# Kernel optimization log

Measured on AMD Instinct MI355X. Metric: run time of the kernel, lower is better.

Reference implementation:

```python
import jax, jax.numpy as jnp
import numpy as np

B, H, T, K, V = 2, 8, 2048, 128, 128


def setup_inputs() -> dict:
    key = jax.random.key(0)
    k1, k2, k3, k4, k5 = jax.random.split(key, 5)
    return {
        "q": jax.random.normal(k1, (B, H, T, K), dtype=jnp.float32),
        "k": jax.random.normal(k2, (B, H, T, K), dtype=jnp.float32),
        "v": jax.random.normal(k3, (B, H, T, V), dtype=jnp.float32),
        "i_gate": jax.random.normal(k4, (B, H, T), dtype=jnp.float32),
        "f_gate": jax.random.normal(k5, (B, H, T), dtype=jnp.float32),
    }


def reference(q, k, v, i_gate, f_gate):
    # Stabilized parallel mLSTM (same math as the chunked Triton kernel,
    # expressed in natural-log base instead of base-2).
    Bq, Hq, Tq, Kd = q.shape
    scale = Kd ** -0.5
    logf = jax.nn.log_sigmoid(f_gate)                      # [B,H,T]
    fc = jnp.cumsum(logf, axis=-1)                         # cumulative forget logits
    # log decay matrix: logD[t,s] = i[s] + (fc[t] - fc[s]) for s <= t
    logD = fc[..., :, None] - fc[..., None, :] + i_gate[..., None, :]  # [B,H,T,T]
    mask = jnp.tril(jnp.ones((Tq, Tq), dtype=bool))
    logD_masked = jnp.where(mask, logD, -jnp.inf)
    m = jnp.max(logD_masked, axis=-1)                      # row-wise stabilizer [B,H,T]
    D = jnp.where(mask, jnp.exp(logD - m[..., None]), 0.0) # stabilized decay matrix
    S = jnp.einsum("bhtk,bhsk->bhts", q, k) * scale * D    # gated scores
    norm = jnp.maximum(jnp.abs(jnp.sum(S, axis=-1)), jnp.exp(-m))  # [B,H,T]
    h = jnp.einsum("bhts,bhsv->bhtv", S, v) / norm[..., None]
    return h
```

## Files before the change

kernel.cpp:

```cpp
#include <hip/hip_runtime.h>

#define T_SEQ 2048
#define DHEAD 128
#define NBH 16
#define SCALE 0.08838834764831845f

typedef unsigned short u16;
typedef unsigned int u32;
typedef u16 u16x4 __attribute__((ext_vector_type(4)));
typedef u16 u16x8 __attribute__((ext_vector_type(8)));
typedef u32 u32x2 __attribute__((ext_vector_type(2)));
typedef short s16x4 __attribute__((ext_vector_type(4)));
typedef __bf16 bf16x8 __attribute__((ext_vector_type(8)));
typedef float f32x4 __attribute__((ext_vector_type(4)));

__device__ __forceinline__ u16 f2bfu(float x) {
  union { float f; unsigned u; } c; c.f = x;
  unsigned u = c.u;
  u = u + 0x7FFFu + ((u >> 16) & 1u);
  return (u16)(u >> 16);
}

__device__ __forceinline__ u32 packbf2(float lo, float hi) {
  return (u32)f2bfu(lo) | ((u32)f2bfu(hi) << 16);
}

__device__ __forceinline__ bf16x8 ldsFrag(const u16* p) {
  u16x8 t = *(const u16x8*)p;
  return __builtin_bit_cast(bf16x8, t);
}

__device__ __forceinline__ f32x4 mfma16x16x16bf16(s16x4 a, s16x4 b, f32x4 c) {
#if __has_builtin(__builtin_amdgcn_mfma_f32_16x16x16bf16_1k)
  return __builtin_amdgcn_mfma_f32_16x16x16bf16_1k(a, b, c, 0, 0, 0);
#else
  asm("v_mfma_f32_16x16x16_bf16 %0, %1, %2, %0" : "+v"(c) : "v"(a), "v"(b));
  return c;
#endif
}

__device__ __forceinline__ void gld_lds16(const void* g, void* l) {
  __builtin_amdgcn_global_load_lds(
      (__attribute__((address_space(1))) const unsigned int*)g,
      (__attribute__((address_space(3))) unsigned int*)l, 16, 0, 0);
}

__global__ __launch_bounds__(1024) void gate_scan_kernel(
    const float* __restrict__ ig, const float* __restrict__ fg,
    float* __restrict__ a_out, float* __restrict__ c_out,
    float* __restrict__ fc_out)
{
  const int bh = blockIdx.x, tid = threadIdx.x;
  const int w = tid >> 6, lane = tid & 63;
  const int base = bh * T_SEQ + tid * 2;
  __shared__ float wsum[16];
  __shared__ float wmax[16];

  const float x0 = fg[base], x1 = fg[base + 1];
  const float ls0 = fminf(x0, 0.f) - log1pf(expf(-fabsf(x0)));
  const float ls1 = fminf(x1, 0.f) - log1pf(expf(-fabsf(x1)));
  const float s = ls0 + ls1;

  float sc = s;
#pragma unroll
  for (int off = 1; off < 64; off <<= 1) {
    const float t = __shfl_up(sc, off, 64);
    if (lane >= off) sc += t;
  }
  if (lane == 63) wsum[w] = sc;
  __syncthreads();
  float wo = 0.f;
#pragma unroll
  for (int i = 0; i < 15; ++i) if (i < w) wo += wsum[i];
  const float excl = wo + (sc - s);
  const float fc0 = excl + ls0;
  const float fc1 = excl + ls0 + ls1;
  fc_out[base] = fc0; fc_out[base + 1] = fc1;
  const float a0 = ig[base] - fc0;
  const float a1 = ig[base + 1] - fc1;
  a_out[base] = a0; a_out[base + 1] = a1;

  const float m = fmaxf(a0, a1);
  float mc = m;
#pragma unroll
  for (int off = 1; off < 64; off <<= 1) {
    const float t = __shfl_up(mc, off, 64);
    if (lane >= off) mc = fmaxf(mc, t);
  }
  if (lane == 63) wmax[w] = mc;
  __syncthreads();
  float wmo = -INFINITY;
#pragma unroll
  for (int i = 0; i < 15; ++i) if (i < w) wmo = fmaxf(wmo, wmax[i]);
  const float prev = __shfl_up(mc, 1, 64);
  float exclm = (lane > 0) ? prev : -INFINITY;
  exclm = fmaxf(exclm, wmo);
  c_out[base] = fmaxf(exclm, a0);
  c_out[base + 1] = fmaxf(exclm, m);
}

__global__ __launch_bounds__(256) void cvt_k_kernel(
    const float* __restrict__ src, const float* __restrict__ ag,
    const float* __restrict__ cg, u16* __restrict__ dst)
{
  const int i = (blockIdx.x * 256 + threadIdx.x) * 4;
  const int bhs = i >> 7;
  const float sc = __expf(ag[bhs] - cg[bhs | 63]);
  const float4 x = *(const float4*)(src + i);
  u16x4 p;
  p[0] = f2bfu(x.x * sc); p[1] = f2bfu(x.y * sc);
  p[2] = f2bfu(x.z * sc); p[3] = f2bfu(x.w * sc);
  *(u16x4*)(dst + i) = p;
}

__global__ __launch_bounds__(256) void cvt_vt_kernel(
    const float* __restrict__ v, u16* __restrict__ vt)
{
  const int bh = blockIdx.y, kt = blockIdx.x, tid = threadIdx.x;
  __shared__ __align__(16) u16 L[128 * 72];
  const int n0 = (tid & 31) * 4, k0 = (tid >> 5) * 8;
  const float* vp = v + ((size_t)bh * T_SEQ + kt * 64 + k0) * DHEAD + n0;
  u16 tv[4][8];
#pragma unroll
  for (int rr = 0; rr < 8; ++rr) {
    const float4 x = *(const float4*)(vp + rr * DHEAD);
    tv[0][rr] = f2bfu(x.x); tv[1][rr] = f2bfu(x.y);
    tv[2][rr] = f2bfu(x.z); tv[3][rr] = f2bfu(x.w);
  }
#pragma unroll
  for (int j = 0; j < 4; ++j) {
    u16x8 p;
#pragma unroll
    for (int rr = 0; rr < 8; ++rr) p[rr] = tv[j][rr];
    *(u16x8*)(&L[(n0 + j) * 72 + k0]) = p;
  }
  __syncthreads();
  const int row = tid >> 1, s0 = (tid & 1) * 32;
  u16* op = vt + ((size_t)bh * DHEAD + row) * T_SEQ + kt * 64 + s0;
#pragma unroll
  for (int i = 0; i < 4; ++i)
    *(u16x8*)(op + i * 8) = *(const u16x8*)(&L[row * 72 + s0 + i * 8]);
}

template <bool FAST>
__global__ __launch_bounds__(1024, 4) void mlstm_fwd_kernel(
    const float* __restrict__ qg, const float* __restrict__ kxg,
    const float* __restrict__ vg,
    const u16* __restrict__ kbf, const u16* __restrict__ vtbf,
    const float* __restrict__ ag, const float* __restrict__ cg,
    const float* __restrict__ fcg, float* __restrict__ out)
{
  const int bx = (int)blockIdx.x;
  const int bh = bx & 15, p = bx >> 4;
  const int tid = (int)threadIdx.x;
  const int w = tid >> 6, lane = tid & 63;
  const int quad = lane >> 4, l16 = lane & 15;
  const int kg = w & 3, rq = w >> 2;

  const int qtA = 31 - p, qtB = p;
  const int nA = qtA + 1;

  __shared__ __align__(16) unsigned char SM[99584];
  u16* Kst = (u16*)SM;
  u16* Vst = (u16*)(SM + 32768);
  float* osh = (float*)(SM + 65536);
  float* rsh = (float*)(SM + 98560);

  const size_t hoff = (size_t)bh * T_SEQ * DHEAD;
  const int goff = bh * T_SEQ;

  bf16x8 qf[4];
  auto loadQ = [&](int lqt) {
    const float* qp = qg + hoff + (size_t)(lqt * 64 + rq * 16 + l16) * DHEAD + quad * 8;
#pragma unroll
    for (int kc = 0; kc < 4; ++kc) {
      const float4 x0 = *(const float4*)(qp + kc * 32);
      const float4 x1 = *(const float4*)(qp + kc * 32 + 4);
      u16x8 t;
      t[0] = f2bfu(x0.x); t[1] = f2bfu(x0.y); t[2] = f2bfu(x0.z); t[3] = f2bfu(x0.w);
      t[4] = f2bfu(x1.x); t[5] = f2bfu(x1.y); t[6] = f2bfu(x1.z); t[7] = f2bfu(x1.w);
      qf[kc] = __builtin_bit_cast(bf16x8, t);
    }
  };

  f32x4 oa[8];
  float rsacc;
  auto zeroAcc = [&]() {
#pragma unroll
    for (int mt = 0; mt < 8; ++mt) oa[mt] = (f32x4){0.f, 0.f, 0.f, 0.f};
    rsacc = 0.f;
  };
  zeroAcc();

  auto stage = [&](int st, int b) {
    u16* KbL = Kst + b * 8192;
    u16* VbL = Vst + b * 8192;
    if (FAST) {
      const u16* ks = kbf + ((size_t)goff + st * 64) * DHEAD;
      const u16* vs = vtbf + (size_t)bh * DHEAD * T_SEQ + st * 64;
      { const int key = tid >> 4; const int db = (tid & 15) ^ (key & 7);
        gld_lds16(ks + (size_t)key * DHEAD + db * 8, KbL + w * 512); }
      { const int n = tid >> 3; const int kb = (tid & 7) ^ (n & 7);
        gld_lds16(vs + (size_t)n * T_SEQ + kb * 8, VbL + w * 512); }
    } else {
      const float ct = cg[goff + st * 64 + 63];
      const float* kp = kxg + hoff + (size_t)(st * 64) * DHEAD;
      const float* vp = vg + hoff + (size_t)(st * 64) * DHEAD;
      { const int key = tid >> 4; const int db = (tid & 15) ^ (key & 7);
        const float sc = __expf(ag[goff + st * 64 + key] - ct);
        const float4 x0 = *(const float4*)(kp + (size_t)key * DHEAD + db * 8);
        const float4 x1 = *(const float4*)(kp + (size_t)key * DHEAD + db * 8 + 4);
        u16x8 pk;
        pk[0] = f2bfu(x0.x * sc); pk[1] = f2bfu(x0.y * sc);
        pk[2] = f2bfu(x0.z * sc); pk[3] = f2bfu(x0.w * sc);
        pk[4] = f2bfu(x1.x * sc); pk[5] = f2bfu(x1.y * sc);
        pk[6] = f2bfu(x1.z * sc); pk[7] = f2bfu(x1.w * sc);
        *(u16x8*)(KbL + tid * 8) = pk; }
      { const int n = tid >> 3; const int kb = (tid & 7) ^ (n & 7);
        u16x8 pw;
#pragma unroll
        for (int rr = 0; rr < 8; ++rr)
          pw[rr] = f2bfu(vp[(size_t)(kb * 8 + rr) * DHEAD + n]);
        *(u16x8*)(VbL + tid * 8) = pw; }
    }
  };

  const int keyA = kg * 16 + l16;
  const int ksw  = l16 & 7;
  const int kbu  = kg * 2 + (quad >> 1);
  const int kofs = (quad & 1) * 4;

  auto computeTile = [&](int cqt, int st, int b, float ccmax) {
    const u16* KbL = Kst + b * 8192;
    const u16* VbL = Vst + b * 8192;

    f32x4 sa = (f32x4){0.f, 0.f, 0.f, 0.f};
#pragma unroll
    for (int kc = 0; kc < 4; ++kc) {
      const bf16x8 kf = ldsFrag(KbL + keyA * 128 + (((kc * 4 + quad) ^ ksw) * 8));
      sa = __builtin_amdgcn_mfma_f32_16x16x32_bf16(kf, qf[kc], sa, 0, 0, 0);
    }

    const float etile = SCALE * __expf(cg[goff + st * 64 + 63] - ccmax);
    float x0 = sa[0] * etile, x1 = sa[1] * etile;
    float x2 = sa[2] * etile, x3 = sa[3] * etile;
    if (st == cqt) {
      const int qr = rq * 16 + l16, kb0 = kg * 16 + quad * 4;
      if (kb0 + 0 > qr) x0 = 0.f;
      if (kb0 + 1 > qr) x1 = 0.f;
      if (kb0 + 2 > qr) x2 = 0.f;
      if (kb0 + 3 > qr) x3 = 0.f;
    }
    rsacc += (x0 + x1) + (x2 + x3);
    const s16x4 pfr = __builtin_bit_cast(s16x4, (u32x2){packbf2(x0, x1), packbf2(x2, x3)});

#pragma unroll
    for (int mt = 0; mt < 8; ++mt) {
      const int vd = mt * 16 + l16;
      const s16x4 va = *(const s16x4*)(VbL + vd * 64 + ((kbu ^ (vd & 7)) * 8) + kofs);
      oa[mt] = mfma16x16x16bf16(va, pfr, oa[mt]);
    }
  };

  auto epilogue = [&](int eqt, float ecmax) {
    float x = rsacc;
    x += __shfl_xor(x, 16, 64);
    x += __shfl_xor(x, 32, 64);
    if (lane < 16) rsh[kg * 64 + rq * 16 + lane] = x;
    __syncthreads();
    float inv = 0.f;
    if (kg == 3) {
      const int row = rq * 16 + l16;
      const float tot = rsh[row] + rsh[64 + row] + rsh[128 + row] + rsh[192 + row];
      const float nf = __expf(-(ecmax + fcg[goff + eqt * 64 + row]));
      inv = 1.f / fmaxf(fabsf(tot), nf);
    }
    for (int r = 0; r < 4; ++r) {
      if (kg == r) {
#pragma unroll
        for (int mt = 0; mt < 8; ++mt)
#pragma unroll
          for (int rg = 0; rg < 4; ++rg) {
            const int row = rq * 16 + l16;
            const int vd = mt * 16 + quad * 4 + rg;
            const int ad = row * 129 + vd;
            float v = oa[mt][rg];
            if (r > 0) v += osh[ad];
            if (r == 3) v *= inv;
            osh[ad] = v;
          }
      }
      __syncthreads();
    }
    const int col = tid & 31, r0 = tid >> 5;
#pragma unroll
    for (int i = 0; i < 2; ++i) {
      const int row = r0 + 32 * i;
      const float* lp = osh + row * 129 + col * 4;
      float4 v; v.x = lp[0]; v.y = lp[1]; v.z = lp[2]; v.w = lp[3];
      *(float4*)(out + hoff + (size_t)(eqt * 64 + row) * DHEAD + col * 4) = v;
    }
  };

  int qt = qtA;
  float cmax = cg[goff + qtA * 64 + 63];
  loadQ(qtA);
  stage(0, 0);
  __syncthreads();

  for (int it = 0; it < 33; ++it) {
    if (it < 32) {
      const int nx = it + 1;
      stage((nx < nA) ? nx : nx - nA, nx & 1);
    }
    computeTile(qt, (it < nA) ? it : it - nA, it & 1, cmax);
    __syncthreads();
    if (it == nA - 1) {
      epilogue(qtA, cmax);
      zeroAcc();
      qt = qtB;
      cmax = cg[goff + qtB * 64 + 63];
      loadQ(qtB);
    }
  }
  epilogue(qtB, cmax);
}

extern "C" void kernel_launch(void* const* d_in, const int* in_sizes, int n_in,
                              void* d_out, int out_size, void* d_ws, size_t ws_size,
                              hipStream_t stream) {
  const float* q  = (const float*)d_in[0];
  const float* k  = (const float*)d_in[1];
  const float* v  = (const float*)d_in[2];
  const float* ig = (const float*)d_in[3];
  const float* fg = (const float*)d_in[4];

  const size_t gate_bytes = (size_t)3 * NBH * T_SEQ * sizeof(float);
  const size_t kv_elems   = (size_t)NBH * T_SEQ * DHEAD;
  const bool fast = ws_size >= gate_bytes + 2 * kv_elems * sizeof(u16);

  float* a_ws  = (float*)d_ws;
  float* c_ws  = a_ws + NBH * T_SEQ;
  float* fc_ws = c_ws + NBH * T_SEQ;
  u16* kbf  = (u16*)((char*)d_ws + gate_bytes);
  u16* vtbf = kbf + kv_elems;

  gate_scan_kernel<<<dim3(NBH), dim3(1024), 0, stream>>>(ig, fg, a_ws, c_ws, fc_ws);
  if (fast) {
    cvt_k_kernel<<<dim3((unsigned)(kv_elems / 1024)), dim3(256), 0, stream>>>(
        k, a_ws, c_ws, kbf);
    cvt_vt_kernel<<<dim3(T_SEQ / 64, NBH), dim3(256), 0, stream>>>(v, vtbf);
    mlstm_fwd_kernel<true><<<dim3(256), dim3(1024), 0, stream>>>(
        q, k, v, kbf, vtbf, a_ws, c_ws, fc_ws, (float*)d_out);
  } else {
    mlstm_fwd_kernel<false><<<dim3(256), dim3(1024), 0, stream>>>(
        q, k, v, kbf, vtbf, a_ws, c_ws, fc_ws, (float*)d_out);
  }
}
```

Measured before the change: 147.1 us.

## Process two key stages per iteration with 32-row Q per wave; fuse K/V conversion

The main kernel now splits its 16 waves into two stage groups that each handle a different 64-key stage, and each wave computes 32 query rows (two MFMA tiles) so every K/V fragment loaded from LDS is used twice. Stages are double-buffered in pairs, which halves the number of barrier-separated iterations, and the epilogue reduces across 8 wave groups using the freed staging buffer. The separate K-scaling and V-transpose conversion kernels are merged into one launch. In exchange, accumulator registers double, LDS use grows to about 130KB, and the cross-wave output reduction takes twice as many serialized steps.

```diff
diff --git a/kernel.cpp b/kernel.cpp
--- a/kernel.cpp
+++ b/kernel.cpp
@@ -99,24 +99,28 @@
   c_out[base + 1] = fmaxf(exclm, m);
 }
 
-__global__ __launch_bounds__(256) void cvt_k_kernel(
-    const float* __restrict__ src, const float* __restrict__ ag,
-    const float* __restrict__ cg, u16* __restrict__ dst)
-{
-  const int i = (blockIdx.x * 256 + threadIdx.x) * 4;
-  const int bhs = i >> 7;
-  const float sc = __expf(ag[bhs] - cg[bhs | 63]);
-  const float4 x = *(const float4*)(src + i);
-  u16x4 p;
-  p[0] = f2bfu(x.x * sc); p[1] = f2bfu(x.y * sc);
-  p[2] = f2bfu(x.z * sc); p[3] = f2bfu(x.w * sc);
-  *(u16x4*)(dst + i) = p;
-}
-
-__global__ __launch_bounds__(256) void cvt_vt_kernel(
-    const float* __restrict__ v, u16* __restrict__ vt)
+__global__ __launch_bounds__(256) void cvt_kv_kernel(
+    const float* __restrict__ kk, const float* __restrict__ v,
+    const float* __restrict__ ag, const float* __restrict__ cg,
+    u16* __restrict__ kbf, u16* __restrict__ vt)
 {
   const int bh = blockIdx.y, kt = blockIdx.x, tid = threadIdx.x;
+  {
+    const int r = tid >> 2;
+    const int c0 = (tid & 3) * 32;
+    const int row = kt * 64 + r;
+    const float sc = __expf(ag[bh * T_SEQ + row] - cg[bh * T_SEQ + (row | 63)]);
+    const float* sp = kk + ((size_t)bh * T_SEQ + row) * DHEAD + c0;
+    u16* dp = kbf + ((size_t)bh * T_SEQ + row) * DHEAD + c0;
+#pragma unroll
+    for (int j = 0; j < 8; ++j) {
+      const float4 x = *(const float4*)(sp + j * 4);
+      u16x4 pq;
+      pq[0] = f2bfu(x.x * sc); pq[1] = f2bfu(x.y * sc);
+      pq[2] = f2bfu(x.z * sc); pq[3] = f2bfu(x.w * sc);
+      *(u16x4*)(dp + j * 4) = pq;
+    }
+  }
   __shared__ __align__(16) u16 L[128 * 72];
   const int n0 = (tid & 31) * 4, k0 = (tid >> 5) * 8;
   const float* vp = v + ((size_t)bh * T_SEQ + kt * 64 + k0) * DHEAD + n0;
@@ -129,10 +133,10 @@
   }
 #pragma unroll
   for (int j = 0; j < 4; ++j) {
-    u16x8 p;
-#pragma unroll
-    for (int rr = 0; rr < 8; ++rr) p[rr] = tv[j][rr];
-    *(u16x8*)(&L[(n0 + j) * 72 + k0]) = p;
+    u16x8 pq;
+#pragma unroll
+    for (int rr = 0; rr < 8; ++rr) pq[rr] = tv[j][rr];
+    *(u16x8*)(&L[(n0 + j) * 72 + k0]) = pq;
   }
   __syncthreads();
   const int row = tid >> 1, s0 = (tid & 1) * 32;
@@ -155,46 +159,48 @@
   const int tid = (int)threadIdx.x;
   const int w = tid >> 6, lane = tid & 63;
   const int quad = lane >> 4, l16 = lane & 15;
-  const int kg = w & 3, rq = w >> 2;
+  const int kg = w & 3, sg = (w >> 2) & 1, rh = w >> 3;
 
   const int qtA = 31 - p, qtB = p;
-  const int nA = qtA + 1;
-
-  __shared__ __align__(16) unsigned char SM[99584];
-  u16* Kst = (u16*)SM;
-  u16* Vst = (u16*)(SM + 32768);
-  float* osh = (float*)(SM + 65536);
-  float* rsh = (float*)(SM + 98560);
+
+  __shared__ __align__(16) unsigned char SM[133376];
+  float* rsh = (float*)(SM + 131072);
+  float* ish = (float*)(SM + 133120);
 
   const size_t hoff = (size_t)bh * T_SEQ * DHEAD;
   const int goff = bh * T_SEQ;
 
-  bf16x8 qf[4];
+  bf16x8 qf[8];
   auto loadQ = [&](int lqt) {
-    const float* qp = qg + hoff + (size_t)(lqt * 64 + rq * 16 + l16) * DHEAD + quad * 8;
-#pragma unroll
-    for (int kc = 0; kc < 4; ++kc) {
-      const float4 x0 = *(const float4*)(qp + kc * 32);
-      const float4 x1 = *(const float4*)(qp + kc * 32 + 4);
-      u16x8 t;
-      t[0] = f2bfu(x0.x); t[1] = f2bfu(x0.y); t[2] = f2bfu(x0.z); t[3] = f2bfu(x0.w);
-      t[4] = f2bfu(x1.x); t[5] = f2bfu(x1.y); t[6] = f2bfu(x1.z); t[7] = f2bfu(x1.w);
-      qf[kc] = __builtin_bit_cast(bf16x8, t);
-    }
-  };
-
-  f32x4 oa[8];
-  float rsacc;
+    const float* qp = qg + hoff + (size_t)(lqt * 64 + rh * 32 + l16) * DHEAD + quad * 8;
+#pragma unroll
+    for (int nt = 0; nt < 2; ++nt)
+#pragma unroll
+      for (int kc = 0; kc < 4; ++kc) {
+        const float4 x0 = *(const float4*)(qp + nt * 16 * DHEAD + kc * 32);
+        const float4 x1 = *(const float4*)(qp + nt * 16 * DHEAD + kc * 32 + 4);
+        u16x8 t;
+        t[0] = f2bfu(x0.x); t[1] = f2bfu(x0.y); t[2] = f2bfu(x0.z); t[3] = f2bfu(x0.w);
+        t[4] = f2bfu(x1.x); t[5] = f2bfu(x1.y); t[6] = f2bfu(x1.z); t[7] = f2bfu(x1.w);
+        qf[nt * 4 + kc] = __builtin_bit_cast(bf16x8, t);
+      }
+  };
+
+  f32x4 oa[8][2];
+  float rs0, rs1;
   auto zeroAcc = [&]() {
 #pragma unroll
-    for (int mt = 0; mt < 8; ++mt) oa[mt] = (f32x4){0.f, 0.f, 0.f, 0.f};
-    rsacc = 0.f;
+    for (int mt = 0; mt < 8; ++mt) {
+      oa[mt][0] = (f32x4){0.f, 0.f, 0.f, 0.f};
+      oa[mt][1] = (f32x4){0.f, 0.f, 0.f, 0.f};
+    }
+    rs0 = 0.f; rs1 = 0.f;
   };
   zeroAcc();
 
-  auto stage = [&](int st, int b) {
-    u16* KbL = Kst + b * 8192;
-    u16* VbL = Vst + b * 8192;
+  auto stage = [&](int st, int slot) {
+    u16* KbL = (u16*)(SM + slot * 32768);
+    u16* VbL = (u16*)(SM + slot * 32768 + 16384);
     if (FAST) {
       const u16* ks = kbf + ((size_t)goff + st * 64) * DHEAD;
       const u16* vs = vtbf + (size_t)bh * DHEAD * T_SEQ + st * 64;
@@ -225,70 +231,106 @@
     }
   };
 
+  auto stagePair = [&](int s0, int lim, int pr) {
+    if (s0 < lim)     stage(s0,     pr * 2);
+    if (s0 + 1 < lim) stage(s0 + 1, pr * 2 + 1);
+  };
+
   const int keyA = kg * 16 + l16;
   const int ksw  = l16 & 7;
   const int kbu  = kg * 2 + (quad >> 1);
   const int kofs = (quad & 1) * 4;
 
-  auto computeTile = [&](int cqt, int st, int b, float ccmax) {
-    const u16* KbL = Kst + b * 8192;
-    const u16* VbL = Vst + b * 8192;
-
-    f32x4 sa = (f32x4){0.f, 0.f, 0.f, 0.f};
+  auto computeStage = [&](int cqt, int st, int slot, float ccmax) {
+    const u16* KbL = (const u16*)(SM + slot * 32768);
+    const u16* VbL = (const u16*)(SM + slot * 32768 + 16384);
+
+    f32x4 sa0 = (f32x4){0.f, 0.f, 0.f, 0.f};
+    f32x4 sa1 = (f32x4){0.f, 0.f, 0.f, 0.f};
 #pragma unroll
     for (int kc = 0; kc < 4; ++kc) {
       const bf16x8 kf = ldsFrag(KbL + keyA * 128 + (((kc * 4 + quad) ^ ksw) * 8));
-      sa = __builtin_amdgcn_mfma_f32_16x16x32_bf16(kf, qf[kc], sa, 0, 0, 0);
+      sa0 = __builtin_amdgcn_mfma_f32_16x16x32_bf16(kf, qf[kc],     sa0, 0, 0, 0);
+      sa1 = __builtin_amdgcn_mfma_f32_16x16x32_bf16(kf, qf[4 + kc], sa1, 0, 0, 0);
     }
 
     const float etile = SCALE * __expf(cg[goff + st * 64 + 63] - ccmax);
-    float x0 = sa[0] * etile, x1 = sa[1] * etile;
-    float x2 = sa[2] * etile, x3 = sa[3] * etile;
-    if (st == cqt) {
-      const int qr = rq * 16 + l16, kb0 = kg * 16 + quad * 4;
-      if (kb0 + 0 > qr) x0 = 0.f;
-      if (kb0 + 1 > qr) x1 = 0.f;
-      if (kb0 + 2 > qr) x2 = 0.f;
-      if (kb0 + 3 > qr) x3 = 0.f;
-    }
-    rsacc += (x0 + x1) + (x2 + x3);
-    const s16x4 pfr = __builtin_bit_cast(s16x4, (u32x2){packbf2(x0, x1), packbf2(x2, x3)});
+    const bool diag = (st == cqt);
+    const int kb0 = kg * 16 + quad * 4;
+
+    s16x4 pfr0, pfr1;
+    {
+      float x0 = sa0[0] * etile, x1 = sa0[1] * etile;
+      float x2 = sa0[2] * etile, x3 = sa0[3] * etile;
+      if (diag) {
+        const int qr = rh * 32 + l16;
+        if (kb0 + 0 > qr) x0 = 0.f;
+        if (kb0 + 1 > qr) x1 = 0.f;
+        if (kb0 + 2 > qr) x2 = 0.f;
+        if (kb0 + 3 > qr) x3 = 0.f;
+      }
+      rs0 += (x0 + x1) + (x2 + x3);
+      pfr0 = __builtin_bit_cast(s16x4, (u32x2){packbf2(x0, x1), packbf2(x2, x3)});
+    }
+    {
+      float x0 = sa1[0] * etile, x1 = sa1[1] * etile;
+      float x2 = sa1[2] * etile, x3 = sa1[3] * etile;
+      if (diag) {
+        const int qr = rh * 32 + 16 + l16;
+        if (kb0 + 0 > qr) x0 = 0.f;
+        if (kb0 + 1 > qr) x1 = 0.f;
+        if (kb0 + 2 > qr) x2 = 0.f;
+        if (kb0 + 3 > qr) x3 = 0.f;
+      }
+      rs1 += (x0 + x1) + (x2 + x3);
+      pfr1 = __builtin_bit_cast(s16x4, (u32x2){packbf2(x0, x1), packbf2(x2, x3)});
+    }
 
 #pragma unroll
     for (int mt = 0; mt < 8; ++mt) {
       const int vd = mt * 16 + l16;
       const s16x4 va = *(const s16x4*)(VbL + vd * 64 + ((kbu ^ (vd & 7)) * 8) + kofs);
-      oa[mt] = mfma16x16x16bf16(va, pfr, oa[mt]);
-    }
-  };
-
-  auto epilogue = [&](int eqt, float ecmax) {
-    float x = rsacc;
-    x += __shfl_xor(x, 16, 64);
-    x += __shfl_xor(x, 32, 64);
-    if (lane < 16) rsh[kg * 64 + rq * 16 + lane] = x;
+      oa[mt][0] = mfma16x16x16bf16(va, pfr0, oa[mt][0]);
+      oa[mt][1] = mfma16x16x16bf16(va, pfr1, oa[mt][1]);
+    }
+  };
+
+  auto epilogue = [&](int eqt, float ecmax, int epair) {
+    float* osh = (float*)(SM + epair * 65536);
+    float x0 = rs0, x1 = rs1;
+    x0 += __shfl_xor(x0, 16, 64); x0 += __shfl_xor(x0, 32, 64);
+    x1 += __shfl_xor(x1, 16, 64); x1 += __shfl_xor(x1, 32, 64);
+    if (lane < 16) {
+      rsh[(w & 7) * 64 + rh * 32 + lane]      = x0;
+      rsh[(w & 7) * 64 + rh * 32 + 16 + lane] = x1;
+    }
     __syncthreads();
-    float inv = 0.f;
-    if (kg == 3) {
-      const int row = rq * 16 + l16;
-      const float tot = rsh[row] + rsh[64 + row] + rsh[128 + row] + rsh[192 + row];
+    if (w == 15) {
+      const int row = lane;
+      float tot = 0.f;
+#pragma unroll
+      for (int j = 0; j < 8; ++j) tot += rsh[j * 64 + row];
       const float nf = __expf(-(ecmax + fcg[goff + eqt * 64 + row]));
-      inv = 1.f / fmaxf(fabsf(tot), nf);
-    }
-    for (int r = 0; r < 4; ++r) {
-      if (kg == r) {
+      ish[row] = 1.f / fmaxf(fabsf(tot), nf);
+    }
+    for (int r = 0; r < 8; ++r) {
+      if ((w & 7) == r) {
+        float iv0 = 0.f, iv1 = 0.f;
+        if (r == 7) { iv0 = ish[rh * 32 + l16]; iv1 = ish[rh * 32 + 16 + l16]; }
 #pragma unroll
         for (int mt = 0; mt < 8; ++mt)
 #pragma unroll
-          for (int rg = 0; rg < 4; ++rg) {
-            const int row = rq * 16 + l16;
-            const int vd = mt * 16 + quad * 4 + rg;
-            const int ad = row * 129 + vd;
-            float v = oa[mt][rg];
-            if (r > 0) v += osh[ad];
-            if (r == 3) v *= inv;
-            osh[ad] = v;
-          }
+          for (int nt = 0; nt < 2; ++nt)
+#pragma unroll
+            for (int rg = 0; rg < 4; ++rg) {
+              const int row = rh * 32 + nt * 16 + l16;
+              const int vd = mt * 16 + quad * 4 + rg;
+              const int ad = row * 129 + vd;
+              float vv = oa[mt][nt][rg];
+              if (r > 0) vv += osh[ad];
+              if (r == 7) vv *= (nt ? iv1 : iv0);
+              osh[ad] = vv;
+            }
       }
       __syncthreads();
     }
@@ -297,33 +339,37 @@
     for (int i = 0; i < 2; ++i) {
       const int row = r0 + 32 * i;
       const float* lp = osh + row * 129 + col * 4;
-      float4 v; v.x = lp[0]; v.y = lp[1]; v.z = lp[2]; v.w = lp[3];
-      *(float4*)(out + hoff + (size_t)(eqt * 64 + row) * DHEAD + col * 4) = v;
-    }
-  };
-
-  int qt = qtA;
+      float4 vv; vv.x = lp[0]; vv.y = lp[1]; vv.z = lp[2]; vv.w = lp[3];
+      *(float4*)(out + hoff + (size_t)(eqt * 64 + row) * DHEAD + col * 4) = vv;
+    }
+    __syncthreads();
+  };
+
+  int qt = qtA, n = qtA + 1;
   float cmax = cg[goff + qtA * 64 + 63];
   loadQ(qtA);
-  stage(0, 0);
+  stagePair(0, n, 0);
   __syncthreads();
 
-  for (int it = 0; it < 33; ++it) {
-    if (it < 32) {
-      const int nx = it + 1;
-      stage((nx < nA) ? nx : nx - nA, nx & 1);
-    }
-    computeTile(qt, (it < nA) ? it : it - nA, it & 1, cmax);
-    __syncthreads();
-    if (it == nA - 1) {
-      epilogue(qtA, cmax);
+  int pair = 0;
+  for (int phase = 0; phase < 2; ++phase) {
+    const int c = (n + 1) >> 1;
+    for (int g = 0; g < c; ++g) {
+      if (g + 1 < c)        stagePair(2 * (g + 1), n, pair ^ 1);
+      else if (phase == 0)  stagePair(0, qtB + 1, pair ^ 1);
+      const int st = 2 * g + sg;
+      if (st < n) computeStage(qt, st, pair * 2 + sg, cmax);
+      __syncthreads();
+      pair ^= 1;
+    }
+    if (phase == 0) loadQ(qtB);
+    epilogue(qt, cmax, pair ^ 1);
+    if (phase == 0) {
       zeroAcc();
-      qt = qtB;
+      qt = qtB; n = qtB + 1;
       cmax = cg[goff + qtB * 64 + 63];
-      loadQ(qtB);
-    }
-  }
-  epilogue(qtB, cmax);
+    }
+  }
 }
 
 extern "C" void kernel_launch(void* const* d_in, const int* in_sizes, int n_in,
@@ -347,9 +393,8 @@
 
   gate_scan_kernel<<<dim3(NBH), dim3(1024), 0, stream>>>(ig, fg, a_ws, c_ws, fc_ws);
   if (fast) {
-    cvt_k_kernel<<<dim3((unsigned)(kv_elems / 1024)), dim3(256), 0, stream>>>(
-        k, a_ws, c_ws, kbf);
-    cvt_vt_kernel<<<dim3(T_SEQ / 64, NBH), dim3(256), 0, stream>>>(v, vtbf);
+    cvt_kv_kernel<<<dim3(T_SEQ / 64, NBH), dim3(256), 0, stream>>>(
+        k, v, a_ws, c_ws, kbf, vtbf);
     mlstm_fwd_kernel<true><<<dim3(256), dim3(1024), 0, stream>>>(
         q, k, v, kbf, vtbf, a_ws, c_ws, fc_ws, (float*)d_out);
   } else {
```

Result: slower. 196.4 us (+33.5%).

## Triple-buffer K/V staging with vmcnt waits and fuse K/V conversion kernels

Applied to the files above, without the earlier changes.

The main kernel moves from double to triple buffering of K/V tiles in LDS. It waits on vmcnt(2) plus a raw s_barrier, so each iteration needs one barrier instead of two syncthreads and the loads stay two tiles ahead. The K scaling/convert and V transpose kernels are merged into one launch. P packing now uses the hardware v_cvt_pk_bf16_f32 instruction, and the epilogue reduction uses vectorised f32x4 LDS accesses with a 132-float padded row. The cost is larger LDS use (133 KB), which limits occupancy, and the manual waitcnt and barrier handling needs care to stay correct.

```diff
diff --git a/kernel.cpp b/kernel.cpp
--- a/kernel.cpp
+++ b/kernel.cpp
@@ -14,15 +14,13 @@
 typedef __bf16 bf16x8 __attribute__((ext_vector_type(8)));
 typedef float f32x4 __attribute__((ext_vector_type(4)));
 
+#define SFENCE() __builtin_amdgcn_sched_barrier(0)
+
 __device__ __forceinline__ u16 f2bfu(float x) {
   union { float f; unsigned u; } c; c.f = x;
   unsigned u = c.u;
   u = u + 0x7FFFu + ((u >> 16) & 1u);
   return (u16)(u >> 16);
-}
-
-__device__ __forceinline__ u32 packbf2(float lo, float hi) {
-  return (u32)f2bfu(lo) | ((u32)f2bfu(hi) << 16);
 }
 
 __device__ __forceinline__ bf16x8 ldsFrag(const u16* p) {
@@ -99,24 +97,28 @@
   c_out[base + 1] = fmaxf(exclm, m);
 }
 
-__global__ __launch_bounds__(256) void cvt_k_kernel(
-    const float* __restrict__ src, const float* __restrict__ ag,
-    const float* __restrict__ cg, u16* __restrict__ dst)
-{
-  const int i = (blockIdx.x * 256 + threadIdx.x) * 4;
-  const int bhs = i >> 7;
-  const float sc = __expf(ag[bhs] - cg[bhs | 63]);
-  const float4 x = *(const float4*)(src + i);
-  u16x4 p;
-  p[0] = f2bfu(x.x * sc); p[1] = f2bfu(x.y * sc);
-  p[2] = f2bfu(x.z * sc); p[3] = f2bfu(x.w * sc);
-  *(u16x4*)(dst + i) = p;
-}
-
-__global__ __launch_bounds__(256) void cvt_vt_kernel(
-    const float* __restrict__ v, u16* __restrict__ vt)
+__global__ __launch_bounds__(256) void cvt_kv_kernel(
+    const float* __restrict__ kk, const float* __restrict__ v,
+    const float* __restrict__ ag, const float* __restrict__ cg,
+    u16* __restrict__ kbf, u16* __restrict__ vt)
 {
   const int bh = blockIdx.y, kt = blockIdx.x, tid = threadIdx.x;
+  {
+    const int r = tid >> 2;
+    const int c0 = (tid & 3) * 32;
+    const int row = kt * 64 + r;
+    const float sc = __expf(ag[bh * T_SEQ + row] - cg[bh * T_SEQ + (row | 63)]);
+    const float* sp = kk + ((size_t)bh * T_SEQ + row) * DHEAD + c0;
+    u16* dp = kbf + ((size_t)bh * T_SEQ + row) * DHEAD + c0;
+#pragma unroll
+    for (int j = 0; j < 8; ++j) {
+      const float4 x = *(const float4*)(sp + j * 4);
+      u16x4 pq;
+      pq[0] = f2bfu(x.x * sc); pq[1] = f2bfu(x.y * sc);
+      pq[2] = f2bfu(x.z * sc); pq[3] = f2bfu(x.w * sc);
+      *(u16x4*)(dp + j * 4) = pq;
+    }
+  }
   __shared__ __align__(16) u16 L[128 * 72];
   const int n0 = (tid & 31) * 4, k0 = (tid >> 5) * 8;
   const float* vp = v + ((size_t)bh * T_SEQ + kt * 64 + k0) * DHEAD + n0;
@@ -129,10 +131,10 @@
   }
 #pragma unroll
   for (int j = 0; j < 4; ++j) {
-    u16x8 p;
-#pragma unroll
-    for (int rr = 0; rr < 8; ++rr) p[rr] = tv[j][rr];
-    *(u16x8*)(&L[(n0 + j) * 72 + k0]) = p;
+    u16x8 pq;
+#pragma unroll
+    for (int rr = 0; rr < 8; ++rr) pq[rr] = tv[j][rr];
+    *(u16x8*)(&L[(n0 + j) * 72 + k0]) = pq;
   }
   __syncthreads();
   const int row = tid >> 1, s0 = (tid & 1) * 32;
@@ -160,14 +162,20 @@
   const int qtA = 31 - p, qtB = p;
   const int nA = qtA + 1;
 
-  __shared__ __align__(16) unsigned char SM[99584];
+  __shared__ __align__(16) unsigned char SM[133120];
   u16* Kst = (u16*)SM;
-  u16* Vst = (u16*)(SM + 32768);
-  float* osh = (float*)(SM + 65536);
-  float* rsh = (float*)(SM + 98560);
+  float* osh = (float*)(SM + 98304);
+  float* rsh = (float*)(SM + 132096);
 
   const size_t hoff = (size_t)bh * T_SEQ * DHEAD;
   const int goff = bh * T_SEQ;
+
+  auto barL = [&]() {
+    asm volatile("s_waitcnt lgkmcnt(0)" ::: "memory");
+    SFENCE();
+    __builtin_amdgcn_s_barrier();
+    SFENCE();
+  };
 
   bf16x8 qf[4];
   auto loadQ = [&](int lqt) {
@@ -192,47 +200,49 @@
   };
   zeroAcc();
 
-  auto stage = [&](int st, int b) {
-    u16* KbL = Kst + b * 8192;
-    u16* VbL = Vst + b * 8192;
+  const int skey = tid >> 4, sdb = (tid & 15) ^ (skey & 7);
+  const u16* ksBase = kbf + (size_t)goff * DHEAD + (size_t)skey * DHEAD + sdb * 8;
+  const int svn = tid >> 3, svk = (tid & 7) ^ (svn & 7);
+  const u16* vsBase = vtbf + (size_t)bh * DHEAD * T_SEQ + (size_t)svn * T_SEQ + svk * 8;
+
+  auto stage = [&](int st, int slot) {
+    u16* KbL = Kst + slot * 16384;
+    u16* VbL = Kst + slot * 16384 + 8192;
     if (FAST) {
-      const u16* ks = kbf + ((size_t)goff + st * 64) * DHEAD;
-      const u16* vs = vtbf + (size_t)bh * DHEAD * T_SEQ + st * 64;
-      { const int key = tid >> 4; const int db = (tid & 15) ^ (key & 7);
-        gld_lds16(ks + (size_t)key * DHEAD + db * 8, KbL + w * 512); }
-      { const int n = tid >> 3; const int kb = (tid & 7) ^ (n & 7);
-        gld_lds16(vs + (size_t)n * T_SEQ + kb * 8, VbL + w * 512); }
+      gld_lds16(ksBase + (size_t)st * 64 * DHEAD, KbL + w * 512);
+      gld_lds16(vsBase + st * 64, VbL + w * 512);
     } else {
       const float ct = cg[goff + st * 64 + 63];
       const float* kp = kxg + hoff + (size_t)(st * 64) * DHEAD;
       const float* vp = vg + hoff + (size_t)(st * 64) * DHEAD;
-      { const int key = tid >> 4; const int db = (tid & 15) ^ (key & 7);
-        const float sc = __expf(ag[goff + st * 64 + key] - ct);
-        const float4 x0 = *(const float4*)(kp + (size_t)key * DHEAD + db * 8);
-        const float4 x1 = *(const float4*)(kp + (size_t)key * DHEAD + db * 8 + 4);
+      { const float scv = __expf(ag[goff + st * 64 + skey] - ct);
+        const float4 x0 = *(const float4*)(kp + (size_t)skey * DHEAD + sdb * 8);
+        const float4 x1 = *(const float4*)(kp + (size_t)skey * DHEAD + sdb * 8 + 4);
         u16x8 pk;
-        pk[0] = f2bfu(x0.x * sc); pk[1] = f2bfu(x0.y * sc);
-        pk[2] = f2bfu(x0.z * sc); pk[3] = f2bfu(x0.w * sc);
-        pk[4] = f2bfu(x1.x * sc); pk[5] = f2bfu(x1.y * sc);
-        pk[6] = f2bfu(x1.z * sc); pk[7] = f2bfu(x1.w * sc);
+        pk[0] = f2bfu(x0.x * scv); pk[1] = f2bfu(x0.y * scv);
+        pk[2] = f2bfu(x0.z * scv); pk[3] = f2bfu(x0.w * scv);
+        pk[4] = f2bfu(x1.x * scv); pk[5] = f2bfu(x1.y * scv);
+        pk[6] = f2bfu(x1.z * scv); pk[7] = f2bfu(x1.w * scv);
         *(u16x8*)(KbL + tid * 8) = pk; }
-      { const int n = tid >> 3; const int kb = (tid & 7) ^ (n & 7);
-        u16x8 pw;
+      { u16x8 pw;
 #pragma unroll
         for (int rr = 0; rr < 8; ++rr)
-          pw[rr] = f2bfu(vp[(size_t)(kb * 8 + rr) * DHEAD + n]);
+          pw[rr] = f2bfu(vp[(size_t)(svk * 8 + rr) * DHEAD + svn]);
         *(u16x8*)(VbL + tid * 8) = pw; }
     }
+  };
+  auto stageSeq = [&](int seq, int slot) {
+    stage(seq < nA ? seq : seq - nA, slot);
   };
 
   const int keyA = kg * 16 + l16;
   const int ksw  = l16 & 7;
   const int kbu  = kg * 2 + (quad >> 1);
-  const int kofs = (quad & 1) * 4;
-
-  auto computeTile = [&](int cqt, int st, int b, float ccmax) {
-    const u16* KbL = Kst + b * 8192;
-    const u16* VbL = Vst + b * 8192;
+  const int vbase = l16 * 64 + ((kbu ^ (l16 & 7)) * 8) + (quad & 1) * 4;
+
+  auto computeStage = [&](int cqt, int st, int slot, float ccmax) {
+    const u16* KbL = Kst + slot * 16384;
+    const u16* VbL = Kst + slot * 16384 + 8192;
 
     f32x4 sa = (f32x4){0.f, 0.f, 0.f, 0.f};
 #pragma unroll
@@ -252,12 +262,14 @@
       if (kb0 + 3 > qr) x3 = 0.f;
     }
     rsacc += (x0 + x1) + (x2 + x3);
-    const s16x4 pfr = __builtin_bit_cast(s16x4, (u32x2){packbf2(x0, x1), packbf2(x2, x3)});
+    u32 plo, phi;
+    asm("v_cvt_pk_bf16_f32 %0, %1, %2" : "=v"(plo) : "v"(x0), "v"(x1));
+    asm("v_cvt_pk_bf16_f32 %0, %1, %2" : "=v"(phi) : "v"(x2), "v"(x3));
+    const s16x4 pfr = __builtin_bit_cast(s16x4, (u32x2){plo, phi});
 
 #pragma unroll
     for (int mt = 0; mt < 8; ++mt) {
-      const int vd = mt * 16 + l16;
-      const s16x4 va = *(const s16x4*)(VbL + vd * 64 + ((kbu ^ (vd & 7)) * 8) + kofs);
+      const s16x4 va = *(const s16x4*)(VbL + vbase + mt * 1024);
       oa[mt] = mfma16x16x16bf16(va, pfr, oa[mt]);
     }
   };
@@ -267,7 +279,7 @@
     x += __shfl_xor(x, 16, 64);
     x += __shfl_xor(x, 32, 64);
     if (lane < 16) rsh[kg * 64 + rq * 16 + lane] = x;
-    __syncthreads();
+    barL();
     float inv = 0.f;
     if (kg == 3) {
       const int row = rq * 16 + l16;
@@ -277,51 +289,57 @@
     }
     for (int r = 0; r < 4; ++r) {
       if (kg == r) {
-#pragma unroll
-        for (int mt = 0; mt < 8; ++mt)
-#pragma unroll
-          for (int rg = 0; rg < 4; ++rg) {
-            const int row = rq * 16 + l16;
-            const int vd = mt * 16 + quad * 4 + rg;
-            const int ad = row * 129 + vd;
-            float v = oa[mt][rg];
-            if (r > 0) v += osh[ad];
-            if (r == 3) v *= inv;
-            osh[ad] = v;
-          }
+        const int row = rq * 16 + l16;
+#pragma unroll
+        for (int mt = 0; mt < 8; ++mt) {
+          float* ap = osh + row * 132 + mt * 16 + quad * 4;
+          f32x4 vv = oa[mt];
+          if (r > 0) vv = vv + *(const f32x4*)ap;
+          if (r == 3) vv = vv * inv;
+          *(f32x4*)ap = vv;
+        }
       }
-      __syncthreads();
+      barL();
     }
     const int col = tid & 31, r0 = tid >> 5;
 #pragma unroll
     for (int i = 0; i < 2; ++i) {
       const int row = r0 + 32 * i;
-      const float* lp = osh + row * 129 + col * 4;
-      float4 v; v.x = lp[0]; v.y = lp[1]; v.z = lp[2]; v.w = lp[3];
-      *(float4*)(out + hoff + (size_t)(eqt * 64 + row) * DHEAD + col * 4) = v;
+      const f32x4 vv = *(const f32x4*)(osh + row * 132 + col * 4);
+      *(f32x4*)(out + hoff + (size_t)(eqt * 64 + row) * DHEAD + col * 4) = vv;
     }
   };
 
   int qt = qtA;
   float cmax = cg[goff + qtA * 64 + 63];
   loadQ(qtA);
-  stage(0, 0);
-  __syncthreads();
-
-  for (int it = 0; it < 33; ++it) {
-    if (it < 32) {
-      const int nx = it + 1;
-      stage((nx < nA) ? nx : nx - nA, nx & 1);
-    }
-    computeTile(qt, (it < nA) ? it : it - nA, it & 1, cmax);
-    __syncthreads();
-    if (it == nA - 1) {
+  stageSeq(0, 0);
+  stageSeq(1, 1);
+
+  int sl = 0;
+  for (int s = 0; s < 33; ++s) {
+    if (s < 32) { asm volatile("s_waitcnt vmcnt(2)" ::: "memory"); }
+    else        { asm volatile("s_waitcnt vmcnt(0)" ::: "memory"); }
+    if (!FAST)  { asm volatile("s_waitcnt lgkmcnt(0)" ::: "memory"); }
+    SFENCE();
+    __builtin_amdgcn_s_barrier();
+    SFENCE();
+
+    if (s + 2 < 33) {
+      const int sl2 = (sl >= 1) ? sl - 1 : 2;
+      stageSeq(s + 2, sl2);
+    }
+    const int stq = (s < nA) ? s : s - nA;
+    computeStage(qt, stq, sl, cmax);
+
+    if (s == nA - 1) {
+      loadQ(qtB);
       epilogue(qtA, cmax);
       zeroAcc();
       qt = qtB;
       cmax = cg[goff + qtB * 64 + 63];
-      loadQ(qtB);
-    }
+    }
+    sl = (sl == 2) ? 0 : sl + 1;
   }
   epilogue(qtB, cmax);
 }
@@ -347,9 +365,8 @@
 
   gate_scan_kernel<<<dim3(NBH), dim3(1024), 0, stream>>>(ig, fg, a_ws, c_ws, fc_ws);
   if (fast) {
-    cvt_k_kernel<<<dim3((unsigned)(kv_elems / 1024)), dim3(256), 0, stream>>>(
-        k, a_ws, c_ws, kbf);
-    cvt_vt_kernel<<<dim3(T_SEQ / 64, NBH), dim3(256), 0, stream>>>(v, vtbf);
+    cvt_kv_kernel<<<dim3(T_SEQ / 64, NBH), dim3(256), 0, stream>>>(
+        k, v, a_ws, c_ws, kbf, vtbf);
     mlstm_fwd_kernel<true><<<dim3(256), dim3(1024), 0, stream>>>(
         q, k, v, kbf, vtbf, a_ws, c_ws, fc_ws, (float*)d_out);
   } else {
```

After: 146.8 us. No clear change (-0.2%).
